# Kernel tuning notes

Hardware: AMD Instinct MI355X
Metric: run time of the kernel (lower is better)

The kernel has to match this reference:

```python
import jax, jax.numpy as jnp
import numpy as np

N = 16      # num_nodes
D = 128     # embedding_dim
H = 8       # num_heads
F = 512     # feedforward_dim
L = 4       # num_layers
IN = 64     # per-node input dim (joint_pos 32 + joint_vel 32)
B = 16384   # batch


def _ln(x, g, b):
    m = x.mean(-1, keepdims=True)
    v = ((x - m) ** 2).mean(-1, keepdims=True)
    return (x - m) * jax.lax.rsqrt(v + 1e-5) * g + b


def setup_inputs() -> dict:
    key = jax.random.key(0)
    ks = jax.random.split(key, 24)
    s = 0.02
    inp = {
        'joint_pos': jax.random.normal(ks[0], (B, 32), jnp.float32),
        'joint_vel': jax.random.normal(ks[1], (B, 32), jnp.float32),
        'adjacency': jax.random.randint(ks[2], (N, N), 0, 2).astype(jnp.int32),
        # per-node embedder (distinct Linear per node, stacked)
        'embed_W': jax.random.normal(ks[3], (N, IN, D), jnp.float32) * s,
        'embed_b': jnp.zeros((N, D), jnp.float32),
        'pos_emb': jax.random.normal(ks[4], (N, D), jnp.float32) * s,
        # per-layer attention params, stacked over layer dim
        'Wq': jax.random.normal(ks[5], (L, D, D), jnp.float32) * s,
        'bq': jnp.zeros((L, D), jnp.float32),
        'Wk': jax.random.normal(ks[6], (L, D, D), jnp.float32) * s,
        'bk': jnp.zeros((L, D), jnp.float32),
        'Wv': jax.random.normal(ks[7], (L, D, D), jnp.float32) * s,
        'bv': jnp.zeros((L, D), jnp.float32),
        'Wo': jax.random.normal(ks[8], (L, D, D), jnp.float32) * s,
        'bo': jnp.zeros((L, D), jnp.float32),
        'ln1_g': jnp.ones((L, D), jnp.float32),
        'ln1_b': jnp.zeros((L, D), jnp.float32),
        'ln2_g': jnp.ones((L, D), jnp.float32),
        'ln2_b': jnp.zeros((L, D), jnp.float32),
        'W1': jax.random.normal(ks[9], (L, D, F), jnp.float32) * s,
        'b1': jnp.zeros((L, F), jnp.float32),
        'W2': jax.random.normal(ks[10], (L, F, D), jnp.float32) * s,
        'b2': jnp.zeros((L, D), jnp.float32),
    }
    return inp


def reference(joint_pos, joint_vel, adjacency, embed_W, embed_b, pos_emb,
              Wq, bq, Wk, bk, Wv, bv, Wo, bo,
              ln1_g, ln1_b, ln2_g, ln2_b, W1, b1, W2, b2):
    # adjacency with forced self-loops -> additive attention mask [N, N]
    adj = adjacency.astype(bool) | jnp.eye(N, dtype=bool)
    mask = jnp.where(adj, 0.0, -jnp.inf).astype(jnp.float32)

    # every node sees the full concatenated obs (list-variant obs_node_dict)
    feats = jnp.concatenate([joint_pos, joint_vel], axis=-1)        # [B, IN]
    # distinct per-node linear embedders, batched as one einsum
    x = jnp.einsum('bi,nio->bno', feats, embed_W) + embed_b + pos_emb  # [B, N, D]

    dh = D // H
    scale = 1.0 / (dh ** 0.5)
    for l in range(L):  # BoT-Hard: mask on every layer; pre-LN
        h = _ln(x, ln1_g[l], ln1_b[l])
        q = (h @ Wq[l] + bq[l]).reshape(-1, N, H, dh)
        k = (h @ Wk[l] + bk[l]).reshape(-1, N, H, dh)
        v = (h @ Wv[l] + bv[l]).reshape(-1, N, H, dh)
        s = jnp.einsum('bnhd,bmhd->bhnm', q, k) * scale + mask       # [B, H, N, N]
        a = jax.nn.softmax(s, axis=-1)
        o = jnp.einsum('bhnm,bmhd->bnhd', a, v).reshape(-1, N, D)
        x = x + o @ Wo[l] + bo[l]
        h2 = _ln(x, ln2_g[l], ln2_b[l])
        x = x + jax.nn.relu(h2 @ W1[l] + b1[l]) @ W2[l] + b2[l]
    return x
```

## Files before the change

### kernel.cpp

```cpp
#include <hip/hip_runtime.h>
#include <stdint.h>

typedef __bf16 bf16;
typedef bf16 bf16x8 __attribute__((ext_vector_type(8)));
typedef bf16 bf16x4 __attribute__((ext_vector_type(4)));
typedef float f32x4 __attribute__((ext_vector_type(4)));
typedef uint32_t u32;
typedef uint8_t u8;

#define B_TOT 16384
#define SWG 4
#define NWGS (B_TOT / SWG)

__device__ __forceinline__ f32x4 mfma32(bf16x8 a, bf16x8 b, f32x4 c) {
  return __builtin_amdgcn_mfma_f32_16x16x32_bf16(a, b, c, 0, 0, 0);
}
__device__ __forceinline__ bf16x8 zero8() {
  bf16x8 v;
#pragma unroll
  for (int j = 0; j < 8; j++) v[j] = (bf16)0.f;
  return v;
}

__device__ __forceinline__ void bar_lg() {
  __builtin_amdgcn_sched_barrier(0);
  asm volatile("s_waitcnt lgkmcnt(0)" ::: "memory");
  __builtin_amdgcn_s_barrier();
  __builtin_amdgcn_sched_barrier(0);
}
__device__ __forceinline__ void bar_v0() {
  __builtin_amdgcn_sched_barrier(0);
  asm volatile("s_waitcnt vmcnt(0) lgkmcnt(0)" ::: "memory");
  __builtin_amdgcn_s_barrier();
  __builtin_amdgcn_sched_barrier(0);
}
__device__ __forceinline__ void bar_v4() {
  __builtin_amdgcn_sched_barrier(0);
  asm volatile("s_waitcnt vmcnt(4) lgkmcnt(0)" ::: "memory");
  __builtin_amdgcn_s_barrier();
  __builtin_amdgcn_sched_barrier(0);
}

__device__ __forceinline__ void stage16(const u8* __restrict__ src, int rowstride, int colbase,
                                        u8* dst, int tid) {
  __builtin_amdgcn_sched_barrier(0);
#pragma unroll
  for (int rr = 0; rr < 4; ++rr) {
    u32 o = (u32)(rr * 256 + tid) * 16u;
    u32 row = o >> 7, cb = o & 0x7Fu;
    const u8* s = src + (size_t)row * (size_t)rowstride + (size_t)colbase
                      + (size_t)(cb ^ ((row & 7u) << 4));
    __builtin_amdgcn_global_load_lds((const __attribute__((address_space(1))) u32*)s,
                                     (__attribute__((address_space(3))) u32*)(dst + o),
                                     16, 0, 0);
  }
}

__device__ __forceinline__ void st_row(u8* base, int row, int col, bf16 v) {
  *(bf16*)(base + (u32)(row * 256) + (u32)((2 * col) ^ ((row & 15) << 4))) = v;
}

__device__ __forceinline__ void loadA_rm(const u8* R, int g, int c, bf16x8 a[2][4]) {
  const u32 sw = (u32)c << 4;
#pragma unroll
  for (int mt = 0; mt < 2; ++mt)
#pragma unroll
    for (int ks = 0; ks < 4; ++ks)
      a[mt][ks] = *(const bf16x8*)(R + (u32)((mt * 16 + c) * 256)
                                     + (((u32)(ks * 64 + g * 16)) ^ sw));
}

__device__ __forceinline__ void gemm_half(const u8* Wb, int khalf, const bf16x8 a[2][4],
                                          f32x4 acc[2][4], int nh, int g, int c) {
  const u32 sw = (u32)(c & 7) << 4;
#pragma unroll
  for (int ksl = 0; ksl < 2; ++ksl) {
    int ks = khalf * 2 + ksl;
#pragma unroll
    for (int nt = 0; nt < 4; ++nt) {
      bf16x8 b = *(const bf16x8*)(Wb + (u32)((nh * 64 + nt * 16 + c) * 128)
                                     + (((u32)(ksl * 64 + g * 16)) ^ sw));
      acc[0][nt] = mfma32(a[0][ks], b, acc[0][nt]);
      acc[1][nt] = mfma32(a[1][ks], b, acc[1][nt]);
    }
  }
}

template <bool RELU>
__device__ __forceinline__ void epi_rm(const f32x4 acc[2][4], const float* __restrict__ bias,
                                       u8* Rdst, int nh, int g, int c) {
#pragma unroll
  for (int nt = 0; nt < 4; ++nt) {
    int col = nh * 64 + nt * 16 + c;
    float bb = bias[col];
#pragma unroll
    for (int mt = 0; mt < 2; ++mt)
#pragma unroll
      for (int r = 0; r < 4; ++r) {
        float v = acc[mt][nt][r] + bb;
        if (RELU) v = fmaxf(v, 0.f);
        st_row(Rdst, mt * 16 + 4 * g + r, col, (bf16)v);
      }
  }
}

__device__ __forceinline__ void pack4(const f32x4 v, u32& w0, u32& w1) {
  union { bf16 h[2]; u32 u; } t0, t1;
  t0.h[0] = (bf16)v[0]; t0.h[1] = (bf16)v[1];
  t1.h[0] = (bf16)v[2]; t1.h[1] = (bf16)v[3];
  w0 = t0.u; w1 = t1.u;
}

__device__ __forceinline__ bf16x8 Rfrag(u32 w0, u32 w1, int g, int c) {
  int s0 = 32 * g + c;
  int s1 = 32 * g + 16 + c;
  u32 a0 = (u32)__shfl((int)w0, s0);
  u32 a1 = (u32)__shfl((int)w1, s0);
  u32 a2 = (u32)__shfl((int)w0, s1);
  u32 a3 = (u32)__shfl((int)w1, s1);
  union { u32 u[4]; bf16x8 v; } r;
  bool ok = (g < 2);
  r.u[0] = ok ? a0 : 0u; r.u[1] = ok ? a1 : 0u;
  r.u[2] = ok ? a2 : 0u; r.u[3] = ok ? a3 : 0u;
  return r.v;
}

__device__ __forceinline__ void ln_part(const f32x4 x[2][4], float sS[2][4], float sS2[2][4]) {
#pragma unroll
  for (int mt = 0; mt < 2; ++mt) {
    f32x4 a = {0.f, 0.f, 0.f, 0.f}, b = {0.f, 0.f, 0.f, 0.f};
#pragma unroll
    for (int nt = 0; nt < 4; ++nt) { a += x[mt][nt]; b += x[mt][nt] * x[mt][nt]; }
#pragma unroll
    for (int r = 0; r < 4; ++r) {
      float s = a[r], s2 = b[r];
#pragma unroll
      for (int off = 1; off < 16; off <<= 1) { s += __shfl_xor(s, off); s2 += __shfl_xor(s2, off); }
      sS[mt][r] = s; sS2[mt][r] = s2;
    }
  }
}

__global__ void __launch_bounds__(256, 2)
bot_main(const int* __restrict__ adj,
         const float* __restrict__ embB, const float* __restrict__ posE,
         const float* __restrict__ pbq, const float* __restrict__ pbk,
         const float* __restrict__ pbv, const float* __restrict__ pbo,
         const float* __restrict__ l1g, const float* __restrict__ l1b,
         const float* __restrict__ l2g, const float* __restrict__ l2b,
         const float* __restrict__ pb1, const float* __restrict__ pb2,
         const bf16* __restrict__ feats, const bf16* __restrict__ embWT,
         const bf16* __restrict__ wqT, const bf16* __restrict__ wkT,
         const bf16* __restrict__ wvT, const bf16* __restrict__ woT,
         const bf16* __restrict__ w1T, const bf16* __restrict__ w2T,
         float* __restrict__ out) {
  __shared__ u8 smem[81920];
  const int tid = threadIdx.x;
  const int w = tid >> 6, lane = tid & 63, g = lane >> 4, c = lane & 15;
  const int p = w >> 1, nh = w & 1;
  const int S0 = blockIdx.x * SWG;

  u8* pairb = smem + p * 16384;
  u8* Th = pairb;
  u8* Tq = pairb + 8192;
  u8* WB0 = smem + 32768;
  u8* WB1 = smem + 49152;
  u8* WB2 = smem + 65536;
  float* scr = (float*)Tq;

  float maskT[4];
#pragma unroll
  for (int r = 0; r < 4; ++r) {
    int m = 4 * g + r;
    maskT[r] = (adj[c * 16 + m] != 0 || c == m) ? 0.f : -1e9f;
  }

  {
    float* x0 = (float*)smem;
    bf16x8 af[2];
#pragma unroll
    for (int ks = 0; ks < 2; ++ks)
      af[ks] = *(const bf16x8*)(feats + (size_t)(S0 + (c & 3)) * 64 + ks * 32 + g * 8);
#pragma unroll
    for (int pp = 0; pp < 2; ++pp) {
      f32x4 ea[16] = {};
#pragma unroll
      for (int nt = 0; nt < 16; ++nt) {
#pragma unroll
        for (int ks = 0; ks < 2; ++ks) {
          bf16x8 bw = *(const bf16x8*)(embWT
              + (size_t)(w * 512 + pp * 256 + nt * 16 + c) * 64 + ks * 32 + g * 8);
          ea[nt] = mfma32(af[ks], bw, ea[nt]);
        }
      }
      if (g == 0) {
#pragma unroll
        for (int nt = 0; nt < 16; ++nt)
#pragma unroll
          for (int r = 0; r < 4; ++r)
            x0[r * 2048 + w * 512 + pp * 256 + nt * 16 + c] = ea[nt][r];
      }
    }
  }
  __syncthreads();

  f32x4 x[2][4];
  {
    const float* x0 = (const float*)smem;
#pragma unroll
    for (int nt = 0; nt < 4; ++nt)
#pragma unroll
      for (int r = 0; r < 4; ++r) {
        int n = 4 * g + r, d = nh * 64 + nt * 16 + c;
        float eb = embB[n * 128 + d] + posE[n * 128 + d];
#pragma unroll
        for (int mt = 0; mt < 2; ++mt)
          x[mt][nt][r] = x0[(2 * p + mt) * 2048 + n * 128 + d] + eb;
      }
  }
  __syncthreads();

  bf16x8 Ah[2][4], Ah2[2][4], Au[2][4];

#pragma unroll 1
  for (int l = 0; l < 4; ++l) {
    const u8* Wq_l = (const u8*)(wqT + (size_t)l * 16384);
    const u8* Wk_l = (const u8*)(wkT + (size_t)l * 16384);
    const u8* Wv_l = (const u8*)(wvT + (size_t)l * 16384);
    const u8* Wo_l = (const u8*)(woT + (size_t)l * 16384);
    const u8* W1_l = (const u8*)(w1T + (size_t)l * 65536);
    const u8* W2_l = (const u8*)(w2T + (size_t)l * 65536);

    float sS[2][4], sS2[2][4], mean[2][4], rstd[2][4];

    ln_part(x, sS, sS2);
    if (c == 0) {
#pragma unroll
      for (int mt = 0; mt < 2; ++mt)
#pragma unroll
        for (int r = 0; r < 4; ++r) {
          int row = mt * 16 + 4 * g + r;
          scr[(row * 2 + nh) * 2 + 0] = sS[mt][r];
          scr[(row * 2 + nh) * 2 + 1] = sS2[mt][r];
        }
    }
    stage16(Wq_l, 256, 0, WB0, tid);
    bar_v4();

#pragma unroll
    for (int mt = 0; mt < 2; ++mt)
#pragma unroll
      for (int r = 0; r < 4; ++r) {
        int row = mt * 16 + 4 * g + r;
        float s = sS[mt][r] + scr[(row * 2 + (1 - nh)) * 2 + 0];
        float s2 = sS2[mt][r] + scr[(row * 2 + (1 - nh)) * 2 + 1];
        float mu = s * (1.f / 128.f);
        float va = s2 * (1.f / 128.f) - mu * mu;
        mean[mt][r] = mu; rstd[mt][r] = rsqrtf(va + 1e-5f);
      }
#pragma unroll
    for (int nt = 0; nt < 4; ++nt) {
      int col = nh * 64 + nt * 16 + c;
      float gg = l1g[l * 128 + col], bb = l1b[l * 128 + col];
#pragma unroll
      for (int mt = 0; mt < 2; ++mt)
#pragma unroll
        for (int r = 0; r < 4; ++r)
          st_row(Th, mt * 16 + 4 * g + r, col,
                 (bf16)((x[mt][nt][r] - mean[mt][r]) * rstd[mt][r] * gg + bb));
    }
    stage16(Wq_l, 256, 128, WB1, tid);
    bar_v4();

    f32x4 acc[2][4];
    loadA_rm(Th, g, c, Ah);
#pragma unroll
    for (int mt = 0; mt < 2; ++mt)
#pragma unroll
      for (int nt = 0; nt < 4; ++nt) acc[mt][nt] = (f32x4){0.f, 0.f, 0.f, 0.f};
    gemm_half(WB0, 0, Ah, acc, nh, g, c);
    stage16(Wk_l, 256, 0, WB2, tid);
    bar_v4();

    gemm_half(WB1, 1, Ah, acc, nh, g, c);
    epi_rm<false>(acc, pbq + l * 128, Tq, nh, g, c);
    stage16(Wk_l, 256, 128, WB0, tid);
    bar_v4();

#pragma unroll
    for (int mt = 0; mt < 2; ++mt)
#pragma unroll
      for (int nt = 0; nt < 4; ++nt) acc[mt][nt] = (f32x4){0.f, 0.f, 0.f, 0.f};
    gemm_half(WB2, 0, Ah, acc, nh, g, c);
    stage16(Wv_l, 256, 0, WB1, tid);
    bar_v4();

    gemm_half(WB0, 1, Ah, acc, nh, g, c);
    epi_rm<false>(acc, pbk + l * 128, Th, nh, g, c);
    stage16(Wv_l, 256, 128, WB2, tid);
    bar_v4();

#pragma unroll
    for (int mt = 0; mt < 2; ++mt)
#pragma unroll
      for (int nt = 0; nt < 4; ++nt) acc[mt][nt] = (f32x4){0.f, 0.f, 0.f, 0.f};
    gemm_half(WB1, 0, Ah, acc, nh, g, c);
    bar_v0();

    bf16x8 Vf[2][4];
    gemm_half(WB2, 1, Ah, acc, nh, g, c);
#pragma unroll
    for (int nt = 0; nt < 4; ++nt) {
      float bb = pbv[l * 128 + nh * 64 + nt * 16 + c];
#pragma unroll
      for (int mt = 0; mt < 2; ++mt) {
        f32x4 v;
#pragma unroll
        for (int r = 0; r < 4; ++r) v[r] = acc[mt][nt][r] + bb;
        u32 w0, w1; pack4(v, w0, w1);
        Vf[mt][nt] = Rfrag(w0, w1, g, c);
      }
    }
    stage16(Wo_l, 256, 0, WB0, tid);
    bar_v4();

    {
      const f32x4 zz = {0.f, 0.f, 0.f, 0.f};
      const u32 swa = (u32)c << 4;
#pragma unroll
      for (int hh = 0; hh < 4; ++hh) {
        const int gh = nh * 4 + hh;
        bf16x8 qf[2], kf[2];
#pragma unroll
        for (int mt = 0; mt < 2; ++mt) {
          if (g < 2) {
            qf[mt] = *(const bf16x8*)(Tq + (u32)((mt * 16 + c) * 256)
                                         + (((u32)(gh * 32 + g * 16)) ^ swa));
            kf[mt] = *(const bf16x8*)(Th + (u32)((mt * 16 + c) * 256)
                                         + (((u32)(gh * 32 + g * 16)) ^ swa));
          } else { qf[mt] = zero8(); kf[mt] = zero8(); }
        }
#pragma unroll
        for (int mt = 0; mt < 2; ++mt) {
          f32x4 st = mfma32(kf[mt], qf[mt], zz);
          float pr[4];
#pragma unroll
          for (int r = 0; r < 4; ++r) pr[r] = st[r] * 0.25f + maskT[r];
          float mx = fmaxf(fmaxf(pr[0], pr[1]), fmaxf(pr[2], pr[3]));
          mx = fmaxf(mx, __shfl_xor(mx, 16));
          mx = fmaxf(mx, __shfl_xor(mx, 32));
          float sm = 0.f;
#pragma unroll
          for (int r = 0; r < 4; ++r) { pr[r] = __expf(pr[r] - mx); sm += pr[r]; }
          sm += __shfl_xor(sm, 16);
          sm += __shfl_xor(sm, 32);
          float pinv = __fdividef(1.f, sm);
          f32x4 pv;
#pragma unroll
          for (int r = 0; r < 4; ++r) pv[r] = pr[r] * pinv;
          u32 w0, w1; pack4(pv, w0, w1);
          bf16x8 Pf = Rfrag(w0, w1, g, c);
          f32x4 oo = mfma32(Vf[mt][hh], Pf, zz);
          pack4(oo, w0, w1);
          bf16x8 Of = Rfrag(w0, w1, g, c);
          if (g < 2)
            *(bf16x8*)(Tq + (u32)((mt * 16 + c) * 256)
                          + (((u32)(gh * 32 + g * 16)) ^ swa)) = Of;
        }
      }
    }
    stage16(Wo_l, 256, 128, WB1, tid);
    bar_v4();

    loadA_rm(Tq, g, c, Ah);
    gemm_half(WB0, 0, Ah, x, nh, g, c);
    bar_v0();

    gemm_half(WB1, 1, Ah, x, nh, g, c);
#pragma unroll
    for (int nt = 0; nt < 4; ++nt) {
      float bb = pbo[l * 128 + nh * 64 + nt * 16 + c];
#pragma unroll
      for (int mt = 0; mt < 2; ++mt)
#pragma unroll
        for (int r = 0; r < 4; ++r) x[mt][nt][r] += bb;
    }
    ln_part(x, sS, sS2);
    if (c == 0) {
#pragma unroll
      for (int mt = 0; mt < 2; ++mt)
#pragma unroll
        for (int r = 0; r < 4; ++r) {
          int row = mt * 16 + 4 * g + r;
          scr[(row * 2 + nh) * 2 + 0] = sS[mt][r];
          scr[(row * 2 + nh) * 2 + 1] = sS2[mt][r];
        }
    }
    stage16(W1_l, 256, 0, WB2, tid);
    bar_v4();

#pragma unroll
    for (int mt = 0; mt < 2; ++mt)
#pragma unroll
      for (int r = 0; r < 4; ++r) {
        int row = mt * 16 + 4 * g + r;
        float s = sS[mt][r] + scr[(row * 2 + (1 - nh)) * 2 + 0];
        float s2 = sS2[mt][r] + scr[(row * 2 + (1 - nh)) * 2 + 1];
        float mu = s * (1.f / 128.f);
        float va = s2 * (1.f / 128.f) - mu * mu;
        mean[mt][r] = mu; rstd[mt][r] = rsqrtf(va + 1e-5f);
      }
#pragma unroll
    for (int nt = 0; nt < 4; ++nt) {
      int col = nh * 64 + nt * 16 + c;
      float gg = l2g[l * 128 + col], bb = l2b[l * 128 + col];
#pragma unroll
      for (int mt = 0; mt < 2; ++mt)
#pragma unroll
        for (int r = 0; r < 4; ++r)
          st_row(Th, mt * 16 + 4 * g + r, col,
                 (bf16)((x[mt][nt][r] - mean[mt][r]) * rstd[mt][r] * gg + bb));
    }
    stage16(W1_l, 256, 128, WB0, tid);
    bar_v4();

    u8 *bA = WB2, *bB = WB0, *bC = WB1;
#pragma unroll 1
    for (int fc = 0; fc < 4; ++fc) {
      f32x4 uacc[2][4];
#pragma unroll
      for (int mt = 0; mt < 2; ++mt)
#pragma unroll
        for (int nt = 0; nt < 4; ++nt) uacc[mt][nt] = (f32x4){0.f, 0.f, 0.f, 0.f};
      if (fc == 0) loadA_rm(Th, g, c, Ah2);
      gemm_half(bA, 0, Ah2, uacc, nh, g, c);
      stage16(W2_l, 1024, fc * 256, bC, tid);
      bar_v4();
      gemm_half(bB, 1, Ah2, uacc, nh, g, c);
      epi_rm<true>(uacc, pb1 + l * 512 + fc * 128, Tq, nh, g, c);
      stage16(W2_l, 1024, fc * 256 + 128, bA, tid);
      bar_v4();
      loadA_rm(Tq, g, c, Au);
      gemm_half(bC, 0, Au, x, nh, g, c);
      if (fc < 3) { stage16(W1_l + (fc + 1) * 32768, 256, 0, bB, tid); bar_v4(); }
      else bar_v0();
      gemm_half(bA, 1, Au, x, nh, g, c);
      if (fc < 3) { stage16(W1_l + (fc + 1) * 32768, 256, 128, bC, tid); bar_v4(); }
      else {
#pragma unroll
        for (int nt = 0; nt < 4; ++nt) {
          float bb = pb2[l * 128 + nh * 64 + nt * 16 + c];
#pragma unroll
          for (int mt = 0; mt < 2; ++mt)
#pragma unroll
            for (int r = 0; r < 4; ++r) x[mt][nt][r] += bb;
        }
        bar_lg();
      }
      u8* t = bA; bA = bB; bB = bC; bC = t;
    }
  }

#pragma unroll
  for (int nt = 0; nt < 4; ++nt) {
    int col = nh * 64 + nt * 16 + c;
#pragma unroll
    for (int mt = 0; mt < 2; ++mt)
      *(f32x4*)(pairb + mt * 8192 + col * 64 + g * 16) = x[mt][nt];
  }
  bar_lg();
  {
    const int smp = S0 + 2 * p + nh;
    const u8* src = pairb + nh * 8192;
#pragma unroll
    for (int it = 0; it < 8; ++it) {
      int n = it * 2 + (lane >> 5);
      int slot = lane & 31;
      f32x4 v;
#pragma unroll
      for (int e = 0; e < 4; ++e)
        v[e] = *(const float*)(src + (u32)((slot * 4 + e) * 64 + n * 4));
      *(f32x4*)(out + (size_t)smp * 2048 + n * 128 + slot * 4) = v;
    }
  }
}

__global__ void prep_feats_k(const float* __restrict__ pos, const float* __restrict__ vel,
                             bf16* __restrict__ feats) {
  int i = blockIdx.x * 256 + threadIdx.x;
  if (i >= B_TOT * 64) return;
  int b = i >> 6, k = i & 63;
  float v = (k < 32) ? pos[b * 32 + k] : vel[b * 32 + (k - 32)];
  feats[i] = (bf16)v;
}

__global__ void prep_tr_k(const float* __restrict__ src, bf16* __restrict__ dst,
                          int R, int C, int total) {
  int i = blockIdx.x * 256 + threadIdx.x;
  if (i >= total) return;
  int rc = R * C;
  int m = i / rc, rem = i % rc;
  int cc = rem / R, rr = rem % R;
  dst[i] = (bf16)src[(size_t)m * rc + rr * C + cc];
}

extern "C" void kernel_launch(void* const* d_in, const int* in_sizes, int n_in,
                              void* d_out, int out_size, void* d_ws, size_t ws_size,
                              hipStream_t stream) {
  const float* jp  = (const float*)d_in[0];
  const float* jv  = (const float*)d_in[1];
  const int*   adj = (const int*)d_in[2];
  const float* eW  = (const float*)d_in[3];
  const float* eB  = (const float*)d_in[4];
  const float* pE  = (const float*)d_in[5];
  const float* Wq  = (const float*)d_in[6];  const float* bq = (const float*)d_in[7];
  const float* Wk  = (const float*)d_in[8];  const float* bk = (const float*)d_in[9];
  const float* Wv  = (const float*)d_in[10]; const float* bv = (const float*)d_in[11];
  const float* Wo  = (const float*)d_in[12]; const float* bo = (const float*)d_in[13];
  const float* g1  = (const float*)d_in[14]; const float* be1 = (const float*)d_in[15];
  const float* g2  = (const float*)d_in[16]; const float* be2 = (const float*)d_in[17];
  const float* W1  = (const float*)d_in[18]; const float* b1 = (const float*)d_in[19];
  const float* W2  = (const float*)d_in[20]; const float* b2 = (const float*)d_in[21];

  bf16* ws    = (bf16*)d_ws;
  bf16* feats = ws;
  bf16* embWT = ws + 1048576;
  bf16* wqT   = embWT + 131072;
  bf16* wkT   = wqT + 65536;
  bf16* wvT   = wkT + 65536;
  bf16* woT   = wvT + 65536;
  bf16* w1T   = woT + 65536;
  bf16* w2T   = w1T + 262144;

  prep_feats_k<<<(B_TOT * 64 + 255) / 256, 256, 0, stream>>>(jp, jv, feats);
  prep_tr_k<<<512, 256, 0, stream>>>(eW, embWT, 64, 128, 131072);
  prep_tr_k<<<256, 256, 0, stream>>>(Wq, wqT, 128, 128, 65536);
  prep_tr_k<<<256, 256, 0, stream>>>(Wk, wkT, 128, 128, 65536);
  prep_tr_k<<<256, 256, 0, stream>>>(Wv, wvT, 128, 128, 65536);
  prep_tr_k<<<256, 256, 0, stream>>>(Wo, woT, 128, 128, 65536);
  prep_tr_k<<<1024, 256, 0, stream>>>(W1, w1T, 128, 512, 262144);
  prep_tr_k<<<1024, 256, 0, stream>>>(W2, w2T, 512, 128, 262144);

  bot_main<<<NWGS, 256, 0, stream>>>(adj, eB, pE, bq, bk, bv, bo,
                                     g1, be1, g2, be2, b1, b2,
                                     feats, embWT, wqT, wkT, wvT, woT, w1T, w2T,
                                     (float*)d_out);
}
```

Before: 1.213 ms.

## Read weights directly from global memory and double samples per workgroup

Removes the LDS weight-staging pipeline (global_load_lds into triple buffers with vmcnt barriers). Each GEMM now reads its weight B-fragments straight from global memory, relying on L2/L1 cache hits. The workgroup grows to 512 threads covering 8 samples, and LDS use drops to 64KB so more waves fit per CU. The trade-off is higher global/L1 traffic and unhidden load latency in the inner GEMM loops, and the embedding write loop is reindexed for the larger sample group.

```diff
diff --git a/kernel.cpp b/kernel.cpp
--- a/kernel.cpp
+++ b/kernel.cpp
@@ -9,7 +9,7 @@
 typedef uint8_t u8;
 
 #define B_TOT 16384
-#define SWG 4
+#define SWG 8
 #define NWGS (B_TOT / SWG)
 
 __device__ __forceinline__ f32x4 mfma32(bf16x8 a, bf16x8 b, f32x4 c) {
@@ -28,33 +28,6 @@
   __builtin_amdgcn_s_barrier();
   __builtin_amdgcn_sched_barrier(0);
 }
-__device__ __forceinline__ void bar_v0() {
-  __builtin_amdgcn_sched_barrier(0);
-  asm volatile("s_waitcnt vmcnt(0) lgkmcnt(0)" ::: "memory");
-  __builtin_amdgcn_s_barrier();
-  __builtin_amdgcn_sched_barrier(0);
-}
-__device__ __forceinline__ void bar_v4() {
-  __builtin_amdgcn_sched_barrier(0);
-  asm volatile("s_waitcnt vmcnt(4) lgkmcnt(0)" ::: "memory");
-  __builtin_amdgcn_s_barrier();
-  __builtin_amdgcn_sched_barrier(0);
-}
-
-__device__ __forceinline__ void stage16(const u8* __restrict__ src, int rowstride, int colbase,
-                                        u8* dst, int tid) {
-  __builtin_amdgcn_sched_barrier(0);
-#pragma unroll
-  for (int rr = 0; rr < 4; ++rr) {
-    u32 o = (u32)(rr * 256 + tid) * 16u;
-    u32 row = o >> 7, cb = o & 0x7Fu;
-    const u8* s = src + (size_t)row * (size_t)rowstride + (size_t)colbase
-                      + (size_t)(cb ^ ((row & 7u) << 4));
-    __builtin_amdgcn_global_load_lds((const __attribute__((address_space(1))) u32*)s,
-                                     (__attribute__((address_space(3))) u32*)(dst + o),
-                                     16, 0, 0);
-  }
-}
 
 __device__ __forceinline__ void st_row(u8* base, int row, int col, bf16 v) {
   *(bf16*)(base + (u32)(row * 256) + (u32)((2 * col) ^ ((row & 15) << 4))) = v;
@@ -70,20 +43,18 @@
                                      + (((u32)(ks * 64 + g * 16)) ^ sw));
 }
 
-__device__ __forceinline__ void gemm_half(const u8* Wb, int khalf, const bf16x8 a[2][4],
-                                          f32x4 acc[2][4], int nh, int g, int c) {
-  const u32 sw = (u32)(c & 7) << 4;
-#pragma unroll
-  for (int ksl = 0; ksl < 2; ++ksl) {
-    int ks = khalf * 2 + ksl;
-#pragma unroll
-    for (int nt = 0; nt < 4; ++nt) {
-      bf16x8 b = *(const bf16x8*)(Wb + (u32)((nh * 64 + nt * 16 + c) * 128)
-                                     + (((u32)(ksl * 64 + g * 16)) ^ sw));
+__device__ __forceinline__ void gemm_g(const u8* __restrict__ W, u32 rstride,
+                                       const bf16x8 a[2][4], f32x4 acc[2][4],
+                                       int nh, int g, int c) {
+#pragma unroll
+  for (int ks = 0; ks < 4; ++ks)
+#pragma unroll
+    for (int nt = 0; nt < 4; ++nt) {
+      bf16x8 b = *(const bf16x8*)(W + (size_t)(nh * 64 + nt * 16 + c) * rstride
+                                    + (u32)(ks * 64 + g * 16));
       acc[0][nt] = mfma32(a[0][ks], b, acc[0][nt]);
       acc[1][nt] = mfma32(a[1][ks], b, acc[1][nt]);
     }
-  }
 }
 
 template <bool RELU>
@@ -141,7 +112,7 @@
   }
 }
 
-__global__ void __launch_bounds__(256, 2)
+__global__ void __launch_bounds__(512, 4)
 bot_main(const int* __restrict__ adj,
          const float* __restrict__ embB, const float* __restrict__ posE,
          const float* __restrict__ pbq, const float* __restrict__ pbk,
@@ -154,7 +125,7 @@
          const bf16* __restrict__ wvT, const bf16* __restrict__ woT,
          const bf16* __restrict__ w1T, const bf16* __restrict__ w2T,
          float* __restrict__ out) {
-  __shared__ u8 smem[81920];
+  __shared__ u8 smem[65536];
   const int tid = threadIdx.x;
   const int w = tid >> 6, lane = tid & 63, g = lane >> 4, c = lane & 15;
   const int p = w >> 1, nh = w & 1;
@@ -163,9 +134,6 @@
   u8* pairb = smem + p * 16384;
   u8* Th = pairb;
   u8* Tq = pairb + 8192;
-  u8* WB0 = smem + 32768;
-  u8* WB1 = smem + 49152;
-  u8* WB2 = smem + 65536;
   float* scr = (float*)Tq;
 
   float maskT[4];
@@ -177,29 +145,25 @@
 
   {
     float* x0 = (float*)smem;
+    f32x4 ea[16] = {};
     bf16x8 af[2];
 #pragma unroll
     for (int ks = 0; ks < 2; ++ks)
-      af[ks] = *(const bf16x8*)(feats + (size_t)(S0 + (c & 3)) * 64 + ks * 32 + g * 8);
-#pragma unroll
-    for (int pp = 0; pp < 2; ++pp) {
-      f32x4 ea[16] = {};
-#pragma unroll
-      for (int nt = 0; nt < 16; ++nt) {
-#pragma unroll
-        for (int ks = 0; ks < 2; ++ks) {
-          bf16x8 bw = *(const bf16x8*)(embWT
-              + (size_t)(w * 512 + pp * 256 + nt * 16 + c) * 64 + ks * 32 + g * 8);
-          ea[nt] = mfma32(af[ks], bw, ea[nt]);
-        }
-      }
-      if (g == 0) {
-#pragma unroll
-        for (int nt = 0; nt < 16; ++nt)
-#pragma unroll
-          for (int r = 0; r < 4; ++r)
-            x0[r * 2048 + w * 512 + pp * 256 + nt * 16 + c] = ea[nt][r];
-      }
+      af[ks] = *(const bf16x8*)(feats + (size_t)(S0 + (c & 7)) * 64 + ks * 32 + g * 8);
+#pragma unroll
+    for (int nt = 0; nt < 16; ++nt) {
+#pragma unroll
+      for (int ks = 0; ks < 2; ++ks) {
+        bf16x8 bw = *(const bf16x8*)(embWT + (size_t)(w * 256 + nt * 16 + c) * 64 + ks * 32 + g * 8);
+        ea[nt] = mfma32(af[ks], bw, ea[nt]);
+      }
+    }
+    if (g < 2) {
+#pragma unroll
+      for (int nt = 0; nt < 16; ++nt)
+#pragma unroll
+        for (int r = 0; r < 4; ++r)
+          x0[(4 * g + r) * 2048 + w * 256 + nt * 16 + c] = ea[nt][r];
     }
   }
   __syncthreads();
@@ -244,8 +208,7 @@
           scr[(row * 2 + nh) * 2 + 1] = sS2[mt][r];
         }
     }
-    stage16(Wq_l, 256, 0, WB0, tid);
-    bar_v4();
+    bar_lg();
 
 #pragma unroll
     for (int mt = 0; mt < 2; ++mt)
@@ -269,46 +232,30 @@
           st_row(Th, mt * 16 + 4 * g + r, col,
                  (bf16)((x[mt][nt][r] - mean[mt][r]) * rstd[mt][r] * gg + bb));
     }
-    stage16(Wq_l, 256, 128, WB1, tid);
-    bar_v4();
+    bar_lg();
+
+    loadA_rm(Th, g, c, Ah);
+    bar_lg();
 
     f32x4 acc[2][4];
-    loadA_rm(Th, g, c, Ah);
 #pragma unroll
     for (int mt = 0; mt < 2; ++mt)
 #pragma unroll
       for (int nt = 0; nt < 4; ++nt) acc[mt][nt] = (f32x4){0.f, 0.f, 0.f, 0.f};
-    gemm_half(WB0, 0, Ah, acc, nh, g, c);
-    stage16(Wk_l, 256, 0, WB2, tid);
-    bar_v4();
-
-    gemm_half(WB1, 1, Ah, acc, nh, g, c);
+    gemm_g(Wq_l, 256, Ah, acc, nh, g, c);
     epi_rm<false>(acc, pbq + l * 128, Tq, nh, g, c);
-    stage16(Wk_l, 256, 128, WB0, tid);
-    bar_v4();
-
 #pragma unroll
     for (int mt = 0; mt < 2; ++mt)
 #pragma unroll
       for (int nt = 0; nt < 4; ++nt) acc[mt][nt] = (f32x4){0.f, 0.f, 0.f, 0.f};
-    gemm_half(WB2, 0, Ah, acc, nh, g, c);
-    stage16(Wv_l, 256, 0, WB1, tid);
-    bar_v4();
-
-    gemm_half(WB0, 1, Ah, acc, nh, g, c);
+    gemm_g(Wk_l, 256, Ah, acc, nh, g, c);
     epi_rm<false>(acc, pbk + l * 128, Th, nh, g, c);
-    stage16(Wv_l, 256, 128, WB2, tid);
-    bar_v4();
-
+    bf16x8 Vf[2][4];
 #pragma unroll
     for (int mt = 0; mt < 2; ++mt)
 #pragma unroll
       for (int nt = 0; nt < 4; ++nt) acc[mt][nt] = (f32x4){0.f, 0.f, 0.f, 0.f};
-    gemm_half(WB1, 0, Ah, acc, nh, g, c);
-    bar_v0();
-
-    bf16x8 Vf[2][4];
-    gemm_half(WB2, 1, Ah, acc, nh, g, c);
+    gemm_g(Wv_l, 256, Ah, acc, nh, g, c);
 #pragma unroll
     for (int nt = 0; nt < 4; ++nt) {
       float bb = pbv[l * 128 + nh * 64 + nt * 16 + c];
@@ -321,8 +268,6 @@
         Vf[mt][nt] = Rfrag(w0, w1, g, c);
       }
     }
-    stage16(Wo_l, 256, 0, WB0, tid);
-    bar_v4();
 
     {
       const f32x4 zz = {0.f, 0.f, 0.f, 0.f};
@@ -369,14 +314,12 @@
         }
       }
     }
-    stage16(Wo_l, 256, 128, WB1, tid);
-    bar_v4();
+    bar_lg();
 
     loadA_rm(Tq, g, c, Ah);
-    gemm_half(WB0, 0, Ah, x, nh, g, c);
-    bar_v0();
-
-    gemm_half(WB1, 1, Ah, x, nh, g, c);
+    bar_lg();
+
+    gemm_g(Wo_l, 256, Ah, x, nh, g, c);
 #pragma unroll
     for (int nt = 0; nt < 4; ++nt) {
       float bb = pbo[l * 128 + nh * 64 + nt * 16 + c];
@@ -396,8 +339,7 @@
           scr[(row * 2 + nh) * 2 + 1] = sS2[mt][r];
         }
     }
-    stage16(W1_l, 256, 0, WB2, tid);
-    bar_v4();
+    bar_lg();
 
 #pragma unroll
     for (int mt = 0; mt < 2; ++mt)
@@ -421,10 +363,10 @@
           st_row(Th, mt * 16 + 4 * g + r, col,
                  (bf16)((x[mt][nt][r] - mean[mt][r]) * rstd[mt][r] * gg + bb));
     }
-    stage16(W1_l, 256, 128, WB0, tid);
-    bar_v4();
-
-    u8 *bA = WB2, *bB = WB0, *bC = WB1;
+    bar_lg();
+
+    loadA_rm(Th, g, c, Ah2);
+
 #pragma unroll 1
     for (int fc = 0; fc < 4; ++fc) {
       f32x4 uacc[2][4];
@@ -432,35 +374,24 @@
       for (int mt = 0; mt < 2; ++mt)
 #pragma unroll
         for (int nt = 0; nt < 4; ++nt) uacc[mt][nt] = (f32x4){0.f, 0.f, 0.f, 0.f};
-      if (fc == 0) loadA_rm(Th, g, c, Ah2);
-      gemm_half(bA, 0, Ah2, uacc, nh, g, c);
-      stage16(W2_l, 1024, fc * 256, bC, tid);
-      bar_v4();
-      gemm_half(bB, 1, Ah2, uacc, nh, g, c);
+      gemm_g(W1_l + fc * 32768, 256, Ah2, uacc, nh, g, c);
       epi_rm<true>(uacc, pb1 + l * 512 + fc * 128, Tq, nh, g, c);
-      stage16(W2_l, 1024, fc * 256 + 128, bA, tid);
-      bar_v4();
+      bar_lg();
       loadA_rm(Tq, g, c, Au);
-      gemm_half(bC, 0, Au, x, nh, g, c);
-      if (fc < 3) { stage16(W1_l + (fc + 1) * 32768, 256, 0, bB, tid); bar_v4(); }
-      else bar_v0();
-      gemm_half(bA, 1, Au, x, nh, g, c);
-      if (fc < 3) { stage16(W1_l + (fc + 1) * 32768, 256, 128, bC, tid); bar_v4(); }
-      else {
-#pragma unroll
-        for (int nt = 0; nt < 4; ++nt) {
-          float bb = pb2[l * 128 + nh * 64 + nt * 16 + c];
-#pragma unroll
-          for (int mt = 0; mt < 2; ++mt)
-#pragma unroll
-            for (int r = 0; r < 4; ++r) x[mt][nt][r] += bb;
-        }
-        bar_lg();
-      }
-      u8* t = bA; bA = bB; bB = bC; bC = t;
-    }
-  }
-
+      bar_lg();
+      gemm_g(W2_l + fc * 256, 1024, Au, x, nh, g, c);
+    }
+#pragma unroll
+    for (int nt = 0; nt < 4; ++nt) {
+      float bb = pb2[l * 128 + nh * 64 + nt * 16 + c];
+#pragma unroll
+      for (int mt = 0; mt < 2; ++mt)
+#pragma unroll
+        for (int r = 0; r < 4; ++r) x[mt][nt][r] += bb;
+    }
+  }
+
+  bar_lg();
 #pragma unroll
   for (int nt = 0; nt < 4; ++nt) {
     int col = nh * 64 + nt * 16 + c;
@@ -541,7 +472,7 @@
   prep_tr_k<<<1024, 256, 0, stream>>>(W1, w1T, 128, 512, 262144);
   prep_tr_k<<<1024, 256, 0, stream>>>(W2, w2T, 512, 128, 262144);
 
-  bot_main<<<NWGS, 256, 0, stream>>>(adj, eB, pE, bq, bk, bv, bo,
+  bot_main<<<NWGS, 512, 0, stream>>>(adj, eB, pE, bq, bk, bv, bo,
                                      g1, be1, g2, be2, b1, b2,
                                      feats, embWT, wqT, wkT, wvT, woT, w1T, w2T,
                                      (float*)d_out);
```

Result: slower. 2.724 ms (+124.5%).
